# Kernel tuning notes

Measured on AMD Instinct MI355X. Metric: run time of the kernel, lower is better.

The kernel has to match this reference:

```python
import jax, jax.numpy as jnp
import numpy as np

B, S, W = 32, 256, 32
T = 16               # topics per doc, each spanning L = S//T sentences
VOCAB, E, H, D = 400001, 300, 128, 128


def _gru_scan(x, Wih, Whh, bih, bhh, reverse=False):
    """x: [B,S,E] -> (outputs [B,S,H], final hidden [B,H]). Torch GRU cell math."""
    h0 = jnp.zeros((x.shape[0], Whh.shape[1]), x.dtype)
    gi_all = jnp.einsum('bse,ge->bsg', x, Wih) + bih  # precompute input gates [B,S,3H]

    def step(h, gi):
        gh = h @ Whh.T + bhh
        ir, iz, inn = jnp.split(gi, 3, axis=-1)
        hr, hz, hn = jnp.split(gh, 3, axis=-1)
        r = jax.nn.sigmoid(ir + hr)
        z = jax.nn.sigmoid(iz + hz)
        n = jnp.tanh(inn + r * hn)
        h_new = (1.0 - z) * n + z * h
        return h_new, h_new

    hT, hs = jax.lax.scan(step, h0, jnp.swapaxes(gi_all, 0, 1), reverse=reverse)
    return jnp.swapaxes(hs, 0, 1), hT


def setup_inputs() -> dict:
    key = jax.random.key(0)
    ks = jax.random.split(key, 16)
    sc_i = 1.0 / np.sqrt(H)
    L = S // T
    starts = (jnp.arange(T, dtype=jnp.int32) * L + 1)          # 1-based inclusive
    ends = (jnp.arange(T, dtype=jnp.int32) + 1) * L
    tse = jnp.broadcast_to(jnp.stack([starts, ends], axis=-1)[None], (B, T, 2)).astype(jnp.int32)
    return {
        'word_ids': jax.random.randint(ks[0], (B, S, W), 0, VOCAB, dtype=jnp.int32),
        'topic_start_ends': tse,
        'embed_table': jax.random.normal(ks[1], (VOCAB, E), jnp.float32) * 0.6,
        'Wih_f': jax.random.normal(ks[2], (3 * H, E), jnp.float32) * sc_i,
        'Whh_f': jax.random.normal(ks[3], (3 * H, H), jnp.float32) * sc_i,
        'bih_f': jax.random.normal(ks[4], (3 * H,), jnp.float32) * sc_i,
        'bhh_f': jax.random.normal(ks[5], (3 * H,), jnp.float32) * sc_i,
        'Wih_b': jax.random.normal(ks[6], (3 * H, E), jnp.float32) * sc_i,
        'Whh_b': jax.random.normal(ks[7], (3 * H, H), jnp.float32) * sc_i,
        'bih_b': jax.random.normal(ks[8], (3 * H,), jnp.float32) * sc_i,
        'bhh_b': jax.random.normal(ks[9], (3 * H,), jnp.float32) * sc_i,
        'v_attention': jax.random.normal(ks[10], (4 * H, 1), jnp.float32),
        'W_attention': jax.random.normal(ks[11], (4 * H, 4 * H), jnp.float32) * (1.0 / np.sqrt(4 * H)),
        'W1': jax.random.normal(ks[12], (D, 4 * H), jnp.float32) * (1.0 / np.sqrt(4 * H)),
        'b1': jax.random.normal(ks[13], (D,), jnp.float32) * 0.01,
        'W2': jax.random.normal(ks[14], (1, D), jnp.float32) * (1.0 / np.sqrt(D)),
        'b2': jax.random.normal(ks[15], (1,), jnp.float32) * 0.01,
    }


def reference(word_ids, topic_start_ends, embed_table,
              Wih_f, Whh_f, bih_f, bhh_f, Wih_b, Whh_b, bih_b, bhh_b,
              v_attention, W_attention, W1, b1, W2, b2):
    b, s, _ = word_ids.shape
    h = Whh_f.shape[1]
    # --- sent_encoder: gather word embeddings, mean-pool per sentence ---
    sent_emb = jnp.mean(embed_table[word_ids], axis=2)          # [B,S,E]
    # --- doc_encoder: bi-GRU ---
    out_f, hT_f = _gru_scan(sent_emb, Wih_f, Whh_f, bih_f, bhh_f, reverse=False)
    out_b, hT_b = _gru_scan(sent_emb, Wih_b, Whh_b, bih_b, bhh_b, reverse=True)
    sent_rep = jnp.concatenate([out_f, out_b], axis=-1)         # [B,S,2H]
    # faithful to hidden.view(batch_size, 2H) on hidden of shape [2,B,H]
    doc_vec = jnp.stack([hT_f, hT_b], axis=0).reshape(b, 2 * h)
    doc_rep = jnp.broadcast_to(doc_vec[:, None, :], (b, s, 2 * h))
    # topic reps via segment difference of cumulative GRU states (pad trick)
    pad = jnp.pad(sent_rep, ((0, 0), (1, 1), (0, 0)))           # [B,S+2,2H]
    starts = topic_start_ends[:, :, 0]                          # [B,T], 1-based
    ends = topic_start_ends[:, :, 1]

    def gat(idx, lo, hi):
        return jnp.take_along_axis(pad[..., lo:hi], idx[:, :, None], axis=1)
    fwd_part = gat(ends, 0, h) - gat(starts - 1, 0, h)
    bwd_part = gat(starts, h, 2 * h) - gat(ends + 1, h, 2 * h)
    topic_mat = jnp.concatenate([fwd_part, bwd_part], axis=-1)  # [B,T,2H]
    # scatter topic vectors to sentences: topic id = #starts at or before sentence
    sidx = jnp.arange(s, dtype=starts.dtype)
    topic_id = jnp.sum(sidx[None, :, None] >= (starts - 1)[:, None, :], axis=-1) - 1  # [B,S]
    topic_rep = jnp.take_along_axis(topic_mat, topic_id[:, :, None], axis=1)          # [B,S,2H]
    # --- decoder ---
    cat_ds = jnp.concatenate([doc_rep, sent_rep], axis=-1)      # [B,S,4H]
    cat_ts = jnp.concatenate([topic_rep, sent_rep], axis=-1)
    doc_scores = jnp.tanh(cat_ds @ W_attention) @ v_attention   # [B,S,1]
    topic_scores = jnp.tanh(cat_ts @ W_attention) @ v_attention
    doc_w = jax.nn.softmax(doc_scores, axis=1)
    topic_w = jax.nn.softmax(topic_scores, axis=1)
    context = doc_w * doc_rep + topic_w * topic_rep             # [B,S,2H]
    inp = jnp.concatenate([sent_rep, context], axis=-1)         # [B,S,4H]
    hdd = jax.nn.relu(inp @ W1.T + b1)                          # dropout = identity (eval)
    logits = (hdd @ W2.T + b2).squeeze(-1)                      # [B,S]
    return logits
```

## Files before the change

### kernel.cpp

```cpp
#include <hip/hip_runtime.h>
#include <hip/hip_bf16.h>
#include <cstdint>

#define Bk 32
#define Sk 256
#define Wk 32
#define Tk 16
#define Ek 300
#define Hk 128
#define Dk 128
#define NROWS (Bk*Sk)
#define GI_N  (3*Hk*2)
#define KPAD  320

typedef __attribute__((ext_vector_type(8))) short short8v;
typedef __attribute__((ext_vector_type(4))) float f32x4;

__device__ __forceinline__ float fast_sigmoid(float x) {
    return 1.f / (1.f + __expf(-x));
}
__device__ __forceinline__ float fast_tanh(float x) {
    float ax = fabsf(x);
    float e = __expf(2.f * ax);
    float t = 1.f - 2.f / (1.f + e);
    return copysignf(t, x);
}
__device__ __forceinline__ void barrier_lgkm() {
    asm volatile("s_waitcnt lgkmcnt(0)" ::: "memory");
    __builtin_amdgcn_s_barrier();
}
__device__ __forceinline__ unsigned short f2bf(float f) {
    uint32_t u = __float_as_uint(f);
    uint32_t r = (u + 0x7FFFu + ((u >> 16) & 1u)) >> 16;
    return (unsigned short)r;
}
__device__ __forceinline__ float bf2f(unsigned short h) {
    return __uint_as_float(((uint32_t)h) << 16);
}

__global__ __launch_bounds__(256) void pack_kernel(
    const float* __restrict__ Wf, const float* __restrict__ Wb,
    const float* __restrict__ bf, const float* __restrict__ bb,
    const float* __restrict__ Watt, const float* __restrict__ W1,
    unsigned short* __restrict__ Bgt_hi, unsigned short* __restrict__ Bgt_lo,
    float* __restrict__ bias_gi, unsigned short* __restrict__ Wswt,
    unsigned short* __restrict__ W1H, unsigned short* __restrict__ W1L,
    unsigned short* __restrict__ WatTopH, unsigned short* __restrict__ WatTopL)
{
    int idx = blockIdx.x * 256 + threadIdx.x;
    if (idx < 768 * KPAD) {
        int n = idx / KPAD, k = idx % KPAD;
        float v = 0.f;
        if (k < 300) v = (n < 384) ? Wf[n * 300 + k] : Wb[(n - 384) * 300 + k];
        unsigned short h = f2bf(v);
        Bgt_hi[idx] = h;
        Bgt_lo[idx] = f2bf(v - bf2f(h));
    }
    if (idx < 768) bias_gi[idx] = (idx < 384) ? bf[idx] : bb[idx - 384];
    if (idx < 512 * 256) {
        int n = idx >> 8, k = idx & 255;
        Wswt[idx] = f2bf(Watt[(size_t)(256 + k) * 512 + n]);
        float v = Watt[(size_t)k * 512 + n];
        unsigned short h = f2bf(v);
        WatTopH[idx] = h;
        WatTopL[idx] = f2bf(v - bf2f(h));
    }
    if (idx < 128 * 512) {
        float v = W1[idx];
        unsigned short h = f2bf(v);
        W1H[idx] = h;
        W1L[idx] = f2bf(v - bf2f(h));
    }
}

__global__ __launch_bounds__(256) void embed_mean_kernel(
    const int* __restrict__ wids, const float* __restrict__ table,
    unsigned short* __restrict__ Ahi, unsigned short* __restrict__ Alo)
{
    int wv = (blockIdx.x << 2) + (threadIdx.x >> 6);
    int lane = threadIdx.x & 63;
    if (wv >= NROWS) return;
    const int* idp = wids + (size_t)wv * Wk;
    float4 a0 = {0,0,0,0}, a1 = {0,0,0,0};
    #pragma unroll 4
    for (int w = 0; w < Wk; ++w) {
        int id = idp[w];
        const float4* r4 = reinterpret_cast<const float4*>(table + (size_t)id * Ek);
        float4 v0 = r4[lane];
        a0.x += v0.x; a0.y += v0.y; a0.z += v0.z; a0.w += v0.w;
        if (lane < 11) {
            float4 v1 = r4[64 + lane];
            a1.x += v1.x; a1.y += v1.y; a1.z += v1.z; a1.w += v1.w;
        }
    }
    const float sc = 1.f / 32.f;
    unsigned short* hp = Ahi + (size_t)wv * KPAD;
    unsigned short* lp = Alo + (size_t)wv * KPAD;
    {
        float v[4] = {a0.x*sc, a0.y*sc, a0.z*sc, a0.w*sc};
        ushort4 h, l;
        h.x=f2bf(v[0]); h.y=f2bf(v[1]); h.z=f2bf(v[2]); h.w=f2bf(v[3]);
        l.x=f2bf(v[0]-bf2f(h.x)); l.y=f2bf(v[1]-bf2f(h.y));
        l.z=f2bf(v[2]-bf2f(h.z)); l.w=f2bf(v[3]-bf2f(h.w));
        *reinterpret_cast<ushort4*>(hp + lane*4) = h;
        *reinterpret_cast<ushort4*>(lp + lane*4) = l;
    }
    if (lane < 11) {
        float v[4] = {a1.x*sc, a1.y*sc, a1.z*sc, a1.w*sc};
        ushort4 h, l;
        h.x=f2bf(v[0]); h.y=f2bf(v[1]); h.z=f2bf(v[2]); h.w=f2bf(v[3]);
        l.x=f2bf(v[0]-bf2f(h.x)); l.y=f2bf(v[1]-bf2f(h.y));
        l.z=f2bf(v[2]-bf2f(h.z)); l.w=f2bf(v[3]-bf2f(h.w));
        *reinterpret_cast<ushort4*>(hp + 256 + lane*4) = h;
        *reinterpret_cast<ushort4*>(lp + 256 + lane*4) = l;
    } else if (lane < 16) {
        ushort4 z = {0,0,0,0};
        *reinterpret_cast<ushort4*>(hp + 256 + lane*4) = z;
        *reinterpret_cast<ushort4*>(lp + 256 + lane*4) = z;
    }
}

template<int PASSES, bool BIAS, bool RELU>
__global__ __launch_bounds__(256) void mfma_gemm_kernel(
    const unsigned short* __restrict__ Ahi, const unsigned short* __restrict__ Alo,
    const unsigned short* __restrict__ Bthi, const unsigned short* __restrict__ Btlo,
    const float* __restrict__ bias, float* __restrict__ C,
    int M, int N, int Kp)
{
    __shared__ unsigned short At_h[128][40];
    __shared__ unsigned short Bt_h[128][40];
    __shared__ unsigned short At_l[128][40];
    __shared__ unsigned short Bt_l[128][40];
    const int tid = threadIdx.x;
    const int m0 = blockIdx.x * 128, n0 = blockIdx.y * 128;
    const int lane = tid & 63;
    const int wave = tid >> 6;
    const int wr = (wave >> 1) * 64, wc = (wave & 1) * 64;
    const int l15 = lane & 15, l4 = lane >> 4;
    f32x4 acc[4][4] = {};

    const int srow = tid >> 1;
    const int scol = (tid & 1) * 16;

    for (int k0 = 0; k0 < Kp; k0 += 32) {
        {
            const unsigned short* ag = Ahi + (size_t)(m0 + srow) * Kp + k0 + scol;
            *reinterpret_cast<short8v*>(&At_h[srow][scol])     = *reinterpret_cast<const short8v*>(ag);
            *reinterpret_cast<short8v*>(&At_h[srow][scol + 8]) = *reinterpret_cast<const short8v*>(ag + 8);
            const unsigned short* bg = Bthi + (size_t)(n0 + srow) * Kp + k0 + scol;
            *reinterpret_cast<short8v*>(&Bt_h[srow][scol])     = *reinterpret_cast<const short8v*>(bg);
            *reinterpret_cast<short8v*>(&Bt_h[srow][scol + 8]) = *reinterpret_cast<const short8v*>(bg + 8);
            if (PASSES > 1) {
                const unsigned short* ag2 = Alo + (size_t)(m0 + srow) * Kp + k0 + scol;
                *reinterpret_cast<short8v*>(&At_l[srow][scol])     = *reinterpret_cast<const short8v*>(ag2);
                *reinterpret_cast<short8v*>(&At_l[srow][scol + 8]) = *reinterpret_cast<const short8v*>(ag2 + 8);
                const unsigned short* bg2 = Btlo + (size_t)(n0 + srow) * Kp + k0 + scol;
                *reinterpret_cast<short8v*>(&Bt_l[srow][scol])     = *reinterpret_cast<const short8v*>(bg2);
                *reinterpret_cast<short8v*>(&Bt_l[srow][scol + 8]) = *reinterpret_cast<const short8v*>(bg2 + 8);
            }
        }
        __syncthreads();
        short8v a_h[4], b_h[4], a_l[4], b_l[4];
        #pragma unroll
        for (int f = 0; f < 4; ++f) {
            a_h[f] = *reinterpret_cast<const short8v*>(&At_h[wr + f*16 + l15][l4*8]);
            b_h[f] = *reinterpret_cast<const short8v*>(&Bt_h[wc + f*16 + l15][l4*8]);
            if (PASSES > 1) {
                a_l[f] = *reinterpret_cast<const short8v*>(&At_l[wr + f*16 + l15][l4*8]);
                b_l[f] = *reinterpret_cast<const short8v*>(&Bt_l[wc + f*16 + l15][l4*8]);
            }
        }
        #pragma unroll
        for (int i = 0; i < 4; ++i) {
            #pragma unroll
            for (int j = 0; j < 4; ++j) {
                acc[i][j] = __builtin_amdgcn_mfma_f32_16x16x32_bf16(a_h[i], b_h[j], acc[i][j], 0, 0, 0);
                if (PASSES > 1) {
                    acc[i][j] = __builtin_amdgcn_mfma_f32_16x16x32_bf16(a_l[i], b_h[j], acc[i][j], 0, 0, 0);
                    acc[i][j] = __builtin_amdgcn_mfma_f32_16x16x32_bf16(a_h[i], b_l[j], acc[i][j], 0, 0, 0);
                }
            }
        }
        __syncthreads();
    }
    #pragma unroll
    for (int i = 0; i < 4; ++i) {
        #pragma unroll
        for (int j = 0; j < 4; ++j) {
            int col = n0 + wc + j * 16 + l15;
            float badd = BIAS ? bias[col] : 0.f;
            #pragma unroll
            for (int r = 0; r < 4; ++r) {
                int row = m0 + wr + i * 16 + l4 * 4 + r;
                float v = acc[i][j][r] + badd;
                if (RELU) v = fmaxf(v, 0.f);
                C[(size_t)row * N + col] = v;
            }
        }
    }
}

__global__ __launch_bounds__(256) void mfma_w1_logits_kernel(
    const unsigned short* __restrict__ Ahi, const unsigned short* __restrict__ Alo,
    const unsigned short* __restrict__ Bthi, const unsigned short* __restrict__ Btlo,
    const float* __restrict__ b1, const float* __restrict__ W2,
    const float* __restrict__ b2, float* __restrict__ out)
{
    __shared__ unsigned short At_h[128][40];
    __shared__ unsigned short Bt_h[128][40];
    __shared__ unsigned short At_l[128][40];
    __shared__ unsigned short Bt_l[128][40];
    __shared__ float lpart[128];
    const int Kp = 512;
    const int tid = threadIdx.x;
    const int m0 = blockIdx.x * 128;
    const int lane = tid & 63;
    const int wave = tid >> 6;
    const int wr = (wave >> 1) * 64, wc = (wave & 1) * 64;
    const int l15 = lane & 15, l4 = lane >> 4;
    f32x4 acc[4][4] = {};

    const int srow = tid >> 1;
    const int scol = (tid & 1) * 16;

    for (int k0 = 0; k0 < Kp; k0 += 32) {
        {
            const unsigned short* ag = Ahi + (size_t)(m0 + srow) * Kp + k0 + scol;
            *reinterpret_cast<short8v*>(&At_h[srow][scol])     = *reinterpret_cast<const short8v*>(ag);
            *reinterpret_cast<short8v*>(&At_h[srow][scol + 8]) = *reinterpret_cast<const short8v*>(ag + 8);
            const unsigned short* bg = Bthi + (size_t)srow * Kp + k0 + scol;
            *reinterpret_cast<short8v*>(&Bt_h[srow][scol])     = *reinterpret_cast<const short8v*>(bg);
            *reinterpret_cast<short8v*>(&Bt_h[srow][scol + 8]) = *reinterpret_cast<const short8v*>(bg + 8);
            const unsigned short* ag2 = Alo + (size_t)(m0 + srow) * Kp + k0 + scol;
            *reinterpret_cast<short8v*>(&At_l[srow][scol])     = *reinterpret_cast<const short8v*>(ag2);
            *reinterpret_cast<short8v*>(&At_l[srow][scol + 8]) = *reinterpret_cast<const short8v*>(ag2 + 8);
            const unsigned short* bg2 = Btlo + (size_t)srow * Kp + k0 + scol;
            *reinterpret_cast<short8v*>(&Bt_l[srow][scol])     = *reinterpret_cast<const short8v*>(bg2);
            *reinterpret_cast<short8v*>(&Bt_l[srow][scol + 8]) = *reinterpret_cast<const short8v*>(bg2 + 8);
        }
        __syncthreads();
        short8v a_h[4], b_h[4], a_l[4], b_l[4];
        #pragma unroll
        for (int f = 0; f < 4; ++f) {
            a_h[f] = *reinterpret_cast<const short8v*>(&At_h[wr + f*16 + l15][l4*8]);
            b_h[f] = *reinterpret_cast<const short8v*>(&Bt_h[wc + f*16 + l15][l4*8]);
            a_l[f] = *reinterpret_cast<const short8v*>(&At_l[wr + f*16 + l15][l4*8]);
            b_l[f] = *reinterpret_cast<const short8v*>(&Bt_l[wc + f*16 + l15][l4*8]);
        }
        #pragma unroll
        for (int i = 0; i < 4; ++i) {
            #pragma unroll
            for (int j = 0; j < 4; ++j) {
                acc[i][j] = __builtin_amdgcn_mfma_f32_16x16x32_bf16(a_h[i], b_h[j], acc[i][j], 0, 0, 0);
                acc[i][j] = __builtin_amdgcn_mfma_f32_16x16x32_bf16(a_l[i], b_h[j], acc[i][j], 0, 0, 0);
                acc[i][j] = __builtin_amdgcn_mfma_f32_16x16x32_bf16(a_h[i], b_l[j], acc[i][j], 0, 0, 0);
            }
        }
        __syncthreads();
    }
    float b1v[4], w2v[4];
    #pragma unroll
    for (int j = 0; j < 4; ++j) {
        int col = wc + j * 16 + l15;
        b1v[j] = b1[col];
        w2v[j] = W2[col];
    }
    float lsum[4][4];
    #pragma unroll
    for (int i = 0; i < 4; ++i) {
        #pragma unroll
        for (int r = 0; r < 4; ++r) {
            float s = 0.f;
            #pragma unroll
            for (int j = 0; j < 4; ++j) {
                float v = fmaxf(acc[i][j][r] + b1v[j], 0.f);
                s = fmaf(v, w2v[j], s);
            }
            s += __shfl_xor(s, 1); s += __shfl_xor(s, 2);
            s += __shfl_xor(s, 4); s += __shfl_xor(s, 8);
            lsum[i][r] = s;
        }
    }
    if (wc == 0 && l15 == 0) {
        #pragma unroll
        for (int i = 0; i < 4; ++i)
            #pragma unroll
            for (int r = 0; r < 4; ++r)
                lpart[wr + i * 16 + l4 * 4 + r] = lsum[i][r];
    }
    __syncthreads();
    if (wc == 64 && l15 == 0) {
        float bb2 = b2[0];
        #pragma unroll
        for (int i = 0; i < 4; ++i)
            #pragma unroll
            for (int r = 0; r < 4; ++r) {
                int rl = wr + i * 16 + l4 * 4 + r;
                out[m0 + rl] = lpart[rl] + lsum[i][r] + bb2;
            }
    }
}

__global__ __launch_bounds__(256) void mfma_swscore_kernel(
    const unsigned short* __restrict__ Ahi, const unsigned short* __restrict__ Bthi,
    const float* __restrict__ dptp, const float* __restrict__ vatt,
    const int* __restrict__ tidmap,
    float* __restrict__ dscp, float* __restrict__ tscp)
{
    __shared__ unsigned short At_h[128][40];
    __shared__ unsigned short Bt_h[128][40];
    const int tid = threadIdx.x;
    const int m0 = blockIdx.x * 128, n0 = blockIdx.y * 128;
    const int Kp = 256;
    const int lane = tid & 63;
    const int wave = tid >> 6;
    const int wr = (wave >> 1) * 64, wc = (wave & 1) * 64;
    const int l15 = lane & 15, l4 = lane >> 4;
    f32x4 acc[4][4] = {};

    const int srow = tid >> 1;
    const int scol = (tid & 1) * 16;

    for (int k0 = 0; k0 < Kp; k0 += 32) {
        {
            const unsigned short* ag = Ahi + (size_t)(m0 + srow) * Kp + k0 + scol;
            *reinterpret_cast<short8v*>(&At_h[srow][scol])     = *reinterpret_cast<const short8v*>(ag);
            *reinterpret_cast<short8v*>(&At_h[srow][scol + 8]) = *reinterpret_cast<const short8v*>(ag + 8);
            const unsigned short* bg = Bthi + (size_t)(n0 + srow) * Kp + k0 + scol;
            *reinterpret_cast<short8v*>(&Bt_h[srow][scol])     = *reinterpret_cast<const short8v*>(bg);
            *reinterpret_cast<short8v*>(&Bt_h[srow][scol + 8]) = *reinterpret_cast<const short8v*>(bg + 8);
        }
        __syncthreads();
        short8v a_h[4], b_h[4];
        #pragma unroll
        for (int f = 0; f < 4; ++f) {
            a_h[f] = *reinterpret_cast<const short8v*>(&At_h[wr + f*16 + l15][l4*8]);
            b_h[f] = *reinterpret_cast<const short8v*>(&Bt_h[wc + f*16 + l15][l4*8]);
        }
        #pragma unroll
        for (int i = 0; i < 4; ++i)
            #pragma unroll
            for (int j = 0; j < 4; ++j)
                acc[i][j] = __builtin_amdgcn_mfma_f32_16x16x32_bf16(a_h[i], b_h[j], acc[i][j], 0, 0, 0);
        __syncthreads();
    }
    const int bb = m0 >> 8;
    const float* dpr = dptp + (size_t)bb * 512;
    float vv[4], dpv[4];
    #pragma unroll
    for (int j = 0; j < 4; ++j) {
        int col = n0 + wc + j * 16 + l15;
        vv[j] = vatt[col];
        dpv[j] = dpr[col];
    }
    const int slot = blockIdx.y * 2 + (wc >> 6);
    #pragma unroll
    for (int i = 0; i < 4; ++i) {
        #pragma unroll
        for (int r = 0; r < 4; ++r) {
            int row = m0 + wr + i * 16 + l4 * 4 + r;
            int ti = tidmap[row];
            const float* tpr = dptp + (size_t)(32 + bb * 16 + ti) * 512;
            float sd = 0.f, st = 0.f;
            #pragma unroll
            for (int j = 0; j < 4; ++j) {
                int col = n0 + wc + j * 16 + l15;
                float c = acc[i][j][r];
                sd += fast_tanh(c + dpv[j]) * vv[j];
                st += fast_tanh(c + tpr[col]) * vv[j];
            }
            sd += __shfl_xor(sd, 1); sd += __shfl_xor(sd, 2);
            sd += __shfl_xor(sd, 4); sd += __shfl_xor(sd, 8);
            st += __shfl_xor(st, 1); st += __shfl_xor(st, 2);
            st += __shfl_xor(st, 4); st += __shfl_xor(st, 8);
            if (l15 == 0) {
                dscp[(size_t)row * 8 + slot] = sd;
                tscp[(size_t)row * 8 + slot] = st;
            }
        }
    }
}

__global__ __launch_bounds__(512, 1) void gru_scan_kernel(
    const float* __restrict__ gi,
    const float* __restrict__ Whh_f, const float* __restrict__ Whh_b,
    const float* __restrict__ bhh_f, const float* __restrict__ bhh_b,
    float* __restrict__ sent_rep, unsigned short* __restrict__ srh,
    float* __restrict__ hT)
{
    const int blk = blockIdx.x;
    const int dir = blk >> 5;
    const int b   = blk & 31;
    const int t = threadIdx.x;
    const int lane = t & 63;
    const int w_id = t >> 6;
    const int q = lane >> 4;
    const int m = lane & 15;
    const int j = w_id * 16 + m;
    const float* Whh = dir ? Whh_b : Whh_f;
    const float* bhh = dir ? bhh_b : bhh_f;
    __shared__ float hbufA[144];
    __shared__ float hbufB[144];

    const float* wr0 = Whh + (size_t)j * 128 + 32 * q;
    const float* wr1 = wr0 + 128 * 128;
    const float* wr2 = wr0 + 256 * 128;
    float4 wA0 = *reinterpret_cast<const float4*>(wr0 +  0);
    float4 wA1 = *reinterpret_cast<const float4*>(wr0 +  4);
    float4 wA2 = *reinterpret_cast<const float4*>(wr0 +  8);
    float4 wA3 = *reinterpret_cast<const float4*>(wr0 + 12);
    float4 wA4 = *reinterpret_cast<const float4*>(wr0 + 16);
    float4 wA5 = *reinterpret_cast<const float4*>(wr0 + 20);
    float4 wA6 = *reinterpret_cast<const float4*>(wr0 + 24);
    float4 wA7 = *reinterpret_cast<const float4*>(wr0 + 28);
    float4 wB0 = *reinterpret_cast<const float4*>(wr1 +  0);
    float4 wB1 = *reinterpret_cast<const float4*>(wr1 +  4);
    float4 wB2 = *reinterpret_cast<const float4*>(wr1 +  8);
    float4 wB3 = *reinterpret_cast<const float4*>(wr1 + 12);
    float4 wB4 = *reinterpret_cast<const float4*>(wr1 + 16);
    float4 wB5 = *reinterpret_cast<const float4*>(wr1 + 20);
    float4 wB6 = *reinterpret_cast<const float4*>(wr1 + 24);
    float4 wB7 = *reinterpret_cast<const float4*>(wr1 + 28);
    float4 wC0 = *reinterpret_cast<const float4*>(wr2 +  0);
    float4 wC1 = *reinterpret_cast<const float4*>(wr2 +  4);
    float4 wC2 = *reinterpret_cast<const float4*>(wr2 +  8);
    float4 wC3 = *reinterpret_cast<const float4*>(wr2 + 12);
    float4 wC4 = *reinterpret_cast<const float4*>(wr2 + 16);
    float4 wC5 = *reinterpret_cast<const float4*>(wr2 + 20);
    float4 wC6 = *reinterpret_cast<const float4*>(wr2 + 24);
    float4 wC7 = *reinterpret_cast<const float4*>(wr2 + 28);
    const float br = bhh[j];
    const float bz = bhh[128 + j];
    const float bn = bhh[256 + j];

    if (t < 144) { hbufA[t] = 0.f; hbufB[t] = 0.f; }

    const int ji = 36 * (j >> 5) + (j & 31);
    const float* gbase = gi + (size_t)(b * Sk) * GI_N + dir * 384 + j;
    float hold = 0.f;
    float ar = 0.f, az = 0.f, an_ = 0.f;
    float brr = 0.f, bzz = 0.f, bnn = 0.f;
    {
        const long s0 = dir ? (Sk - 1) : 0;
        const long s1 = dir ? (Sk - 2) : 1;
        const float* g0 = gbase + s0 * GI_N;
        ar = g0[0]; az = g0[128]; an_ = g0[256];
        const float* g1 = gbase + s1 * GI_N;
        brr = g1[0]; bzz = g1[128]; bnn = g1[256];
    }
    __syncthreads();

    #define STEP(RD, WR, SEXPR, GR, GZ, GN, SAVE) { \
        const int s = (SEXPR); \
        const float4* hseg = reinterpret_cast<const float4*>(RD) + 9 * q; \
        float pA = 0.f, pB = 0.f, pC = 0.f; \
        { float4 h4; \
          h4 = hseg[0]; \
          pA=fmaf(wA0.x,h4.x,pA); pA=fmaf(wA0.y,h4.y,pA); pA=fmaf(wA0.z,h4.z,pA); pA=fmaf(wA0.w,h4.w,pA); \
          pB=fmaf(wB0.x,h4.x,pB); pB=fmaf(wB0.y,h4.y,pB); pB=fmaf(wB0.z,h4.z,pB); pB=fmaf(wB0.w,h4.w,pB); \
          pC=fmaf(wC0.x,h4.x,pC); pC=fmaf(wC0.y,h4.y,pC); pC=fmaf(wC0.z,h4.z,pC); pC=fmaf(wC0.w,h4.w,pC); \
          h4 = hseg[1]; \
          pA=fmaf(wA1.x,h4.x,pA); pA=fmaf(wA1.y,h4.y,pA); pA=fmaf(wA1.z,h4.z,pA); pA=fmaf(wA1.w,h4.w,pA); \
          pB=fmaf(wB1.x,h4.x,pB); pB=fmaf(wB1.y,h4.y,pB); pB=fmaf(wB1.z,h4.z,pB); pB=fmaf(wB1.w,h4.w,pB); \
          pC=fmaf(wC1.x,h4.x,pC); pC=fmaf(wC1.y,h4.y,pC); pC=fmaf(wC1.z,h4.z,pC); pC=fmaf(wC1.w,h4.w,pC); \
          h4 = hseg[2]; \
          pA=fmaf(wA2.x,h4.x,pA); pA=fmaf(wA2.y,h4.y,pA); pA=fmaf(wA2.z,h4.z,pA); pA=fmaf(wA2.w,h4.w,pA); \
          pB=fmaf(wB2.x,h4.x,pB); pB=fmaf(wB2.y,h4.y,pB); pB=fmaf(wB2.z,h4.z,pB); pB=fmaf(wB2.w,h4.w,pB); \
          pC=fmaf(wC2.x,h4.x,pC); pC=fmaf(wC2.y,h4.y,pC); pC=fmaf(wC2.z,h4.z,pC); pC=fmaf(wC2.w,h4.w,pC); \
          h4 = hseg[3]; \
          pA=fmaf(wA3.x,h4.x,pA); pA=fmaf(wA3.y,h4.y,pA); pA=fmaf(wA3.z,h4.z,pA); pA=fmaf(wA3.w,h4.w,pA); \
          pB=fmaf(wB3.x,h4.x,pB); pB=fmaf(wB3.y,h4.y,pB); pB=fmaf(wB3.z,h4.z,pB); pB=fmaf(wB3.w,h4.w,pB); \
          pC=fmaf(wC3.x,h4.x,pC); pC=fmaf(wC3.y,h4.y,pC); pC=fmaf(wC3.z,h4.z,pC); pC=fmaf(wC3.w,h4.w,pC); \
          h4 = hseg[4]; \
          pA=fmaf(wA4.x,h4.x,pA); pA=fmaf(wA4.y,h4.y,pA); pA=fmaf(wA4.z,h4.z,pA); pA=fmaf(wA4.w,h4.w,pA); \
          pB=fmaf(wB4.x,h4.x,pB); pB=fmaf(wB4.y,h4.y,pB); pB=fmaf(wB4.z,h4.z,pB); pB=fmaf(wB4.w,h4.w,pB); \
          pC=fmaf(wC4.x,h4.x,pC); pC=fmaf(wC4.y,h4.y,pC); pC=fmaf(wC4.z,h4.z,pC); pC=fmaf(wC4.w,h4.w,pC); \
          h4 = hseg[5]; \
          pA=fmaf(wA5.x,h4.x,pA); pA=fmaf(wA5.y,h4.y,pA); pA=fmaf(wA5.z,h4.z,pA); pA=fmaf(wA5.w,h4.w,pA); \
          pB=fmaf(wB5.x,h4.x,pB); pB=fmaf(wB5.y,h4.y,pB); pB=fmaf(wB5.z,h4.z,pB); pB=fmaf(wB5.w,h4.w,pB); \
          pC=fmaf(wC5.x,h4.x,pC); pC=fmaf(wC5.y,h4.y,pC); pC=fmaf(wC5.z,h4.z,pC); pC=fmaf(wC5.w,h4.w,pC); \
          h4 = hseg[6]; \
          pA=fmaf(wA6.x,h4.x,pA); pA=fmaf(wA6.y,h4.y,pA); pA=fmaf(wA6.z,h4.z,pA); pA=fmaf(wA6.w,h4.w,pA); \
          pB=fmaf(wB6.x,h4.x,pB); pB=fmaf(wB6.y,h4.y,pB); pB=fmaf(wB6.z,h4.z,pB); pB=fmaf(wB6.w,h4.w,pB); \
          pC=fmaf(wC6.x,h4.x,pC); pC=fmaf(wC6.y,h4.y,pC); pC=fmaf(wC6.z,h4.z,pC); pC=fmaf(wC6.w,h4.w,pC); \
          h4 = hseg[7]; \
          pA=fmaf(wA7.x,h4.x,pA); pA=fmaf(wA7.y,h4.y,pA); pA=fmaf(wA7.z,h4.z,pA); pA=fmaf(wA7.w,h4.w,pA); \
          pB=fmaf(wB7.x,h4.x,pB); pB=fmaf(wB7.y,h4.y,pB); pB=fmaf(wB7.z,h4.z,pB); pB=fmaf(wB7.w,h4.w,pB); \
          pC=fmaf(wC7.x,h4.x,pC); pC=fmaf(wC7.y,h4.y,pC); pC=fmaf(wC7.z,h4.z,pC); pC=fmaf(wC7.w,h4.w,pC); } \
        pA += __shfl_xor(pA, 16); pA += __shfl_xor(pA, 32); \
        pB += __shfl_xor(pB, 16); pB += __shfl_xor(pB, 32); \
        pC += __shfl_xor(pC, 16); pC += __shfl_xor(pC, 32); \
        if (q == 0) { \
            float r = fast_sigmoid(GR + pA + br); \
            float z = fast_sigmoid(GZ + pB + bz); \
            float n = fast_tanh(GN + r * (pC + bn)); \
            hold = (1.f - z) * n + z * hold; \
            (WR)[ji] = hold; \
            SAVE = hold; \
            const long sn = dir ? (long)s - 2 : (long)s + 2; \
            const float* gp = gbase + sn * GI_N; \
            GR = gp[0]; GZ = gp[128]; GN = gp[256]; \
        } \
        barrier_lgkm(); \
    }

    for (int step = 0; step < Sk; step += 4) {
        float h0 = 0.f, h1 = 0.f, h2 = 0.f, h3 = 0.f;
        STEP(hbufA, hbufB, dir ? (Sk - 1 - step) : step,       ar, az, an_, h0);
        STEP(hbufB, hbufA, dir ? (Sk - 2 - step) : (step + 1), brr, bzz, bnn, h1);
        STEP(hbufA, hbufB, dir ? (Sk - 3 - step) : (step + 2), ar, az, an_, h2);
        STEP(hbufB, hbufA, dir ? (Sk - 4 - step) : (step + 3), brr, bzz, bnn, h3);
        if (q == 0) {
            const size_t base = (size_t)(b * Sk) * 256 + dir * 128 + j;
            const int sA = dir ? (Sk - 1 - step) : step;
            const int d1 = dir ? -1 : 1;
            sent_rep[base + (size_t)(sA)          * 256] = h0;
            sent_rep[base + (size_t)(sA + d1)     * 256] = h1;
            sent_rep[base + (size_t)(sA + 2 * d1) * 256] = h2;
            sent_rep[base + (size_t)(sA + 3 * d1) * 256] = h3;
            srh[base + (size_t)(sA)          * 256] = f2bf(h0);
            srh[base + (size_t)(sA + d1)     * 256] = f2bf(h1);
            srh[base + (size_t)(sA + 2 * d1) * 256] = f2bf(h2);
            srh[base + (size_t)(sA + 3 * d1) * 256] = f2bf(h3);
        }
    }
    #undef STEP

    if (q == 0) hT[dir * 4096 + b * 128 + j] = hold;
}

__device__ __forceinline__ float4 sr_load_guard(const float* sr, int b, int sidx, int j4) {
    if (sidx < 0 || sidx >= Sk) { float4 z = {0,0,0,0}; return z; }
    return reinterpret_cast<const float4*>(sr)[(size_t)(b * Sk + sidx) * 64 + j4];
}
__global__ __launch_bounds__(64) void prep_kernel(
    const int* __restrict__ tse, const float* __restrict__ sent_rep,
    const float* __restrict__ hT, float* __restrict__ dvtm,
    unsigned short* __restrict__ dvtmH, unsigned short* __restrict__ dvtmL,
    int* __restrict__ tidmap)
{
    const int b = blockIdx.x;
    const int t = blockIdx.y;
    const int j4 = threadIdx.x;
    float4 v;
    int row;
    if (t == 16) {
        int dir = b >> 4;
        int bb = 2 * (b & 15) + (j4 >> 5);
        int jj4 = j4 & 31;
        v = reinterpret_cast<const float4*>(hT)[dir * 1024 + bb * 32 + jj4];
        row = b;
        for (int ss = j4; ss < 256; ss += 64) {
            int ti = 0;
            #pragma unroll
            for (int tt = 1; tt < 16; ++tt) ti += (ss >= tse[b * 32 + tt * 2] - 1) ? 1 : 0;
            tidmap[b * 256 + ss] = ti;
        }
    } else {
        int st = tse[b * 32 + t * 2];
        int en = tse[b * 32 + t * 2 + 1];
        float4 va, vb;
        if (j4 < 32) {
            va = sr_load_guard(sent_rep, b, en - 1, j4);
            vb = sr_load_guard(sent_rep, b, st - 2, j4);
        } else {
            va = sr_load_guard(sent_rep, b, st - 1, j4);
            vb = sr_load_guard(sent_rep, b, en, j4);
        }
        v.x = va.x - vb.x; v.y = va.y - vb.y; v.z = va.z - vb.z; v.w = va.w - vb.w;
        row = 32 + b * 16 + t;
    }
    reinterpret_cast<float4*>(dvtm)[row * 64 + j4] = v;
    ushort4 h, l;
    h.x = f2bf(v.x); h.y = f2bf(v.y); h.z = f2bf(v.z); h.w = f2bf(v.w);
    l.x = f2bf(v.x - bf2f(h.x)); l.y = f2bf(v.y - bf2f(h.y));
    l.z = f2bf(v.z - bf2f(h.z)); l.w = f2bf(v.w - bf2f(h.w));
    *reinterpret_cast<ushort4*>(dvtmH + (size_t)row * 256 + j4 * 4) = h;
    *reinterpret_cast<ushort4*>(dvtmL + (size_t)row * 256 + j4 * 4) = l;
}

__global__ __launch_bounds__(256) void softmax_kernel(
    const float* __restrict__ dscp, const float* __restrict__ tscp,
    float* __restrict__ dsc, float* __restrict__ tsc)
{
    const int b = blockIdx.x, sidx = threadIdx.x;
    const int lane = sidx & 63, wid = sidx >> 6;
    __shared__ float rd[4], rt[4];
    const float4* dp8 = reinterpret_cast<const float4*>(dscp + (size_t)(b * Sk + sidx) * 8);
    const float4* tp8 = reinterpret_cast<const float4*>(tscp + (size_t)(b * Sk + sidx) * 8);
    float4 d0 = dp8[0], d1 = dp8[1], t0 = tp8[0], t1 = tp8[1];
    float d = ((d0.x + d0.y) + (d0.z + d0.w)) + ((d1.x + d1.y) + (d1.z + d1.w));
    float t = ((t0.x + t0.y) + (t0.z + t0.w)) + ((t1.x + t1.y) + (t1.z + t1.w));
    float md = d, mt = t;
    #pragma unroll
    for (int off = 32; off; off >>= 1) {
        md = fmaxf(md, __shfl_xor(md, off));
        mt = fmaxf(mt, __shfl_xor(mt, off));
    }
    if (lane == 0) { rd[wid] = md; rt[wid] = mt; }
    __syncthreads();
    md = fmaxf(fmaxf(rd[0], rd[1]), fmaxf(rd[2], rd[3]));
    mt = fmaxf(fmaxf(rt[0], rt[1]), fmaxf(rt[2], rt[3]));
    float ed = __expf(d - md), et = __expf(t - mt);
    float sd = ed, stt = et;
    #pragma unroll
    for (int off = 32; off; off >>= 1) {
        sd += __shfl_xor(sd, off);
        stt += __shfl_xor(stt, off);
    }
    __syncthreads();
    if (lane == 0) { rd[wid] = sd; rt[wid] = stt; }
    __syncthreads();
    sd = rd[0] + rd[1] + rd[2] + rd[3];
    stt = rt[0] + rt[1] + rt[2] + rt[3];
    dsc[b * Sk + sidx] = ed / sd;
    tsc[b * Sk + sidx] = et / stt;
}

__global__ __launch_bounds__(128) void build_inp_kernel(
    const float* __restrict__ sent_rep, const float* __restrict__ dvtm,
    const float* __restrict__ dw, const float* __restrict__ tw,
    const int* __restrict__ tidmap,
    unsigned short* __restrict__ inpH, unsigned short* __restrict__ inpL)
{
    int row = blockIdx.x;
    int b = row >> 8;
    int f4c = threadIdx.x;
    float4 v;
    if (f4c < 64) {
        v = reinterpret_cast<const float4*>(sent_rep)[(size_t)row * 64 + f4c];
    } else {
        int ti = tidmap[row];
        float dwv = dw[row], twv = tw[row];
        int j4 = f4c - 64;
        float4 dv = reinterpret_cast<const float4*>(dvtm)[b * 64 + j4];
        float4 tm = reinterpret_cast<const float4*>(dvtm)[(32 + b * 16 + ti) * 64 + j4];
        v.x = dwv * dv.x + twv * tm.x;
        v.y = dwv * dv.y + twv * tm.y;
        v.z = dwv * dv.z + twv * tm.z;
        v.w = dwv * dv.w + twv * tm.w;
    }
    ushort4 h, l;
    h.x = f2bf(v.x); h.y = f2bf(v.y); h.z = f2bf(v.z); h.w = f2bf(v.w);
    l.x = f2bf(v.x - bf2f(h.x)); l.y = f2bf(v.y - bf2f(h.y));
    l.z = f2bf(v.z - bf2f(h.z)); l.w = f2bf(v.w - bf2f(h.w));
    *reinterpret_cast<ushort4*>(inpH + (size_t)row * 512 + f4c * 4) = h;
    *reinterpret_cast<ushort4*>(inpL + (size_t)row * 512 + f4c * 4) = l;
}

extern "C" void kernel_launch(void* const* d_in, const int* in_sizes, int n_in,
                              void* d_out, int out_size, void* d_ws, size_t ws_size,
                              hipStream_t stream)
{
    const int*   wids  = (const int*)d_in[0];
    const int*   tse   = (const int*)d_in[1];
    const float* table = (const float*)d_in[2];
    const float* Wihf  = (const float*)d_in[3];
    const float* Whhf  = (const float*)d_in[4];
    const float* bihf  = (const float*)d_in[5];
    const float* bhhf  = (const float*)d_in[6];
    const float* Wihb  = (const float*)d_in[7];
    const float* Whhb  = (const float*)d_in[8];
    const float* bihb  = (const float*)d_in[9];
    const float* bhhb  = (const float*)d_in[10];
    const float* vatt  = (const float*)d_in[11];
    const float* Watt  = (const float*)d_in[12];
    const float* W1    = (const float*)d_in[13];
    const float* b1    = (const float*)d_in[14];
    const float* W2    = (const float*)d_in[15];
    const float* b2    = (const float*)d_in[16];
    float* ws = (float*)d_ws;
    float* out = (float*)d_out;

    unsigned short* Ahi   = (unsigned short*)(ws + 0);
    unsigned short* Alo   = (unsigned short*)(ws + 1310720);
    float* gi             = ws + 2621440;
    float* sent_rep       = ws + 8912896;
    unsigned short* SRhi  = (unsigned short*)(ws + 11010048);
    float* hT             = ws + 12058624;
    float* dvtm           = ws + 12066816;
    float* dptp           = ws + 12206080;
    float* dsc            = ws + 12533760;
    float* tsc            = ws + 12541952;
    unsigned short* BgtH  = (unsigned short*)(ws + 12550144);
    unsigned short* BgtL  = (unsigned short*)(ws + 12673024);
    float* bias_gi        = ws + 12795904;
    unsigned short* Wswt  = (unsigned short*)(ws + 12796672);
    unsigned short* W1H   = (unsigned short*)(ws + 12862208);
    unsigned short* W1L   = (unsigned short*)(ws + 12894976);
    float* dscp           = ws + 12927744;
    float* tscp           = ws + 12993280;
    int*   tidmap         = (int*)(ws + 13058816);
    unsigned short* dvtmH = (unsigned short*)(ws + 13067008);
    unsigned short* dvtmL = (unsigned short*)(ws + 13148928);
    unsigned short* WatTH = (unsigned short*)(ws + 13230848);
    unsigned short* WatTL = (unsigned short*)(ws + 13296384);
    unsigned short* inpH  = (unsigned short*)(ws + 0);
    unsigned short* inpL  = (unsigned short*)(ws + 2097152);

    if (ws_size < (size_t)13361920 * sizeof(float)) return;

    pack_kernel<<<960, 256, 0, stream>>>(Wihf, Wihb, bihf, bihb, Watt, W1,
                                         BgtH, BgtL, bias_gi, Wswt, W1H, W1L,
                                         WatTH, WatTL);
    embed_mean_kernel<<<2048, 256, 0, stream>>>(wids, table, Ahi, Alo);
    mfma_gemm_kernel<3, true, false><<<dim3(64, 6), 256, 0, stream>>>(
        Ahi, Alo, BgtH, BgtL, bias_gi, gi, NROWS, 768, KPAD);
    gru_scan_kernel<<<64, 512, 0, stream>>>(gi, Whhf, Whhb, bhhf, bhhb,
                                            sent_rep, SRhi, hT);
    prep_kernel<<<dim3(32, 17), 64, 0, stream>>>(tse, sent_rep, hT, dvtm,
                                                 dvtmH, dvtmL, tidmap);
    mfma_gemm_kernel<3, false, false><<<dim3(5, 4), 256, 0, stream>>>(
        dvtmH, dvtmL, WatTH, WatTL, nullptr, dptp, 640, 512, 256);
    mfma_swscore_kernel<<<dim3(64, 4), 256, 0, stream>>>(
        SRhi, Wswt, dptp, vatt, tidmap, dscp, tscp);
    softmax_kernel<<<32, 256, 0, stream>>>(dscp, tscp, dsc, tsc);
    build_inp_kernel<<<NROWS, 128, 0, stream>>>(sent_rep, dvtm, dsc, tsc, tidmap, inpH, inpL);
    mfma_w1_logits_kernel<<<dim3(64, 1), 256, 0, stream>>>(
        inpH, inpL, W1H, W1L, b1, W2, b2, out);
}
```

Baseline: 332.6 us.

## Batch GRU recurrence across 16 sequences per block using split-bf16 MFMA

The GRU scan kernel is rewritten so that each of four blocks handles one direction and 16 batch rows. The per-step h·Whh^T product runs on MFMA bf16 instructions, with hi/lo splitting of both h and Whh to keep near-fp32 accuracy. The previous scalar FMA kernel used 64 blocks, one per (direction, batch) pair. The change cuts redundant weight work per step but leaves only four blocks active for the serial 256-step chain, so each step now carries MFMA latency, LDS round trips and strided global gi loads.

```diff
diff --git a/kernel.cpp b/kernel.cpp
--- a/kernel.cpp
+++ b/kernel.cpp
@@ -40,12 +40,14 @@
 
 __global__ __launch_bounds__(256) void pack_kernel(
     const float* __restrict__ Wf, const float* __restrict__ Wb,
+    const float* __restrict__ Whh_f, const float* __restrict__ Whh_b,
     const float* __restrict__ bf, const float* __restrict__ bb,
     const float* __restrict__ Watt, const float* __restrict__ W1,
     unsigned short* __restrict__ Bgt_hi, unsigned short* __restrict__ Bgt_lo,
     float* __restrict__ bias_gi, unsigned short* __restrict__ Wswt,
     unsigned short* __restrict__ W1H, unsigned short* __restrict__ W1L,
-    unsigned short* __restrict__ WatTopH, unsigned short* __restrict__ WatTopL)
+    unsigned short* __restrict__ WatTopH, unsigned short* __restrict__ WatTopL,
+    unsigned short* __restrict__ WhhH, unsigned short* __restrict__ WhhL)
 {
     int idx = blockIdx.x * 256 + threadIdx.x;
     if (idx < 768 * KPAD) {
@@ -70,6 +72,15 @@
         unsigned short h = f2bf(v);
         W1H[idx] = h;
         W1L[idx] = f2bf(v - bf2f(h));
+    }
+    if (idx < 2 * 384 * 128) {
+        int dd = idx / 49152;
+        int rest = idx - dd * 49152;
+        const float* W = dd ? Whh_b : Whh_f;
+        float v = W[rest];
+        unsigned short h = f2bf(v);
+        WhhH[idx] = h;
+        WhhL[idx] = f2bf(v - bf2f(h));
     }
 }
 
@@ -381,152 +392,109 @@
     }
 }
 
-__global__ __launch_bounds__(512, 1) void gru_scan_kernel(
+__global__ __launch_bounds__(512, 1) void gru_scan_mfma_kernel(
     const float* __restrict__ gi,
-    const float* __restrict__ Whh_f, const float* __restrict__ Whh_b,
+    const unsigned short* __restrict__ WhhH, const unsigned short* __restrict__ WhhL,
     const float* __restrict__ bhh_f, const float* __restrict__ bhh_b,
     float* __restrict__ sent_rep, unsigned short* __restrict__ srh,
     float* __restrict__ hT)
 {
-    const int blk = blockIdx.x;
-    const int dir = blk >> 5;
-    const int b   = blk & 31;
+    const int dir  = blockIdx.x >> 1;
+    const int half = blockIdx.x & 1;
     const int t = threadIdx.x;
     const int lane = t & 63;
-    const int w_id = t >> 6;
-    const int q = lane >> 4;
-    const int m = lane & 15;
-    const int j = w_id * 16 + m;
-    const float* Whh = dir ? Whh_b : Whh_f;
+    const int w = t >> 6;
+    const int l15 = lane & 15, l4 = lane >> 4;
+    const int j = w * 16 + l15;
     const float* bhh = dir ? bhh_b : bhh_f;
-    __shared__ float hbufA[144];
-    __shared__ float hbufB[144];
-
-    const float* wr0 = Whh + (size_t)j * 128 + 32 * q;
-    const float* wr1 = wr0 + 128 * 128;
-    const float* wr2 = wr0 + 256 * 128;
-    float4 wA0 = *reinterpret_cast<const float4*>(wr0 +  0);
-    float4 wA1 = *reinterpret_cast<const float4*>(wr0 +  4);
-    float4 wA2 = *reinterpret_cast<const float4*>(wr0 +  8);
-    float4 wA3 = *reinterpret_cast<const float4*>(wr0 + 12);
-    float4 wA4 = *reinterpret_cast<const float4*>(wr0 + 16);
-    float4 wA5 = *reinterpret_cast<const float4*>(wr0 + 20);
-    float4 wA6 = *reinterpret_cast<const float4*>(wr0 + 24);
-    float4 wA7 = *reinterpret_cast<const float4*>(wr0 + 28);
-    float4 wB0 = *reinterpret_cast<const float4*>(wr1 +  0);
-    float4 wB1 = *reinterpret_cast<const float4*>(wr1 +  4);
-    float4 wB2 = *reinterpret_cast<const float4*>(wr1 +  8);
-    float4 wB3 = *reinterpret_cast<const float4*>(wr1 + 12);
-    float4 wB4 = *reinterpret_cast<const float4*>(wr1 + 16);
-    float4 wB5 = *reinterpret_cast<const float4*>(wr1 + 20);
-    float4 wB6 = *reinterpret_cast<const float4*>(wr1 + 24);
-    float4 wB7 = *reinterpret_cast<const float4*>(wr1 + 28);
-    float4 wC0 = *reinterpret_cast<const float4*>(wr2 +  0);
-    float4 wC1 = *reinterpret_cast<const float4*>(wr2 +  4);
-    float4 wC2 = *reinterpret_cast<const float4*>(wr2 +  8);
-    float4 wC3 = *reinterpret_cast<const float4*>(wr2 + 12);
-    float4 wC4 = *reinterpret_cast<const float4*>(wr2 + 16);
-    float4 wC5 = *reinterpret_cast<const float4*>(wr2 + 20);
-    float4 wC6 = *reinterpret_cast<const float4*>(wr2 + 24);
-    float4 wC7 = *reinterpret_cast<const float4*>(wr2 + 28);
-    const float br = bhh[j];
-    const float bz = bhh[128 + j];
-    const float bn = bhh[256 + j];
-
-    if (t < 144) { hbufA[t] = 0.f; hbufB[t] = 0.f; }
-
-    const int ji = 36 * (j >> 5) + (j & 31);
-    const float* gbase = gi + (size_t)(b * Sk) * GI_N + dir * 384 + j;
-    float hold = 0.f;
-    float ar = 0.f, az = 0.f, an_ = 0.f;
-    float brr = 0.f, bzz = 0.f, bnn = 0.f;
+    __shared__ unsigned short hls[2][2][16][152];
+
+    const unsigned short* WH = WhhH + (size_t)dir * 49152;
+    const unsigned short* WL = WhhL + (size_t)dir * 49152;
+    short8v bh0[4], bh1[4], bh2[4], bl0[4], bl1[4], bl2[4];
+    #pragma unroll
+    for (int kt = 0; kt < 4; ++kt) {
+        const size_t ko = (size_t)kt * 32 + l4 * 8;
+        bh0[kt] = *reinterpret_cast<const short8v*>(WH + (size_t)(0 * 128 + j) * 128 + ko);
+        bh1[kt] = *reinterpret_cast<const short8v*>(WH + (size_t)(1 * 128 + j) * 128 + ko);
+        bh2[kt] = *reinterpret_cast<const short8v*>(WH + (size_t)(2 * 128 + j) * 128 + ko);
+        bl0[kt] = *reinterpret_cast<const short8v*>(WL + (size_t)(0 * 128 + j) * 128 + ko);
+        bl1[kt] = *reinterpret_cast<const short8v*>(WL + (size_t)(1 * 128 + j) * 128 + ko);
+        bl2[kt] = *reinterpret_cast<const short8v*>(WL + (size_t)(2 * 128 + j) * 128 + ko);
+    }
+    const float b_r = bhh[j], b_z = bhh[128 + j], b_n = bhh[256 + j];
+
+    for (int i = t; i < 2 * 2 * 16 * 152; i += 512) ((unsigned short*)hls)[i] = 0;
+
+    float giA[12], giB[12];
     {
-        const long s0 = dir ? (Sk - 1) : 0;
-        const long s1 = dir ? (Sk - 2) : 1;
-        const float* g0 = gbase + s0 * GI_N;
-        ar = g0[0]; az = g0[128]; an_ = g0[256];
-        const float* g1 = gbase + s1 * GI_N;
-        brr = g1[0]; bzz = g1[128]; bnn = g1[256];
-    }
+        const int s0 = dir ? (Sk - 1) : 0;
+        const int s1 = dir ? (Sk - 2) : 1;
+        #pragma unroll
+        for (int r = 0; r < 4; ++r) {
+            const int b = half * 16 + l4 * 4 + r;
+            const float* g0 = gi + ((size_t)b * Sk + s0) * GI_N + dir * 384 + j;
+            giA[3*r+0] = g0[0]; giA[3*r+1] = g0[128]; giA[3*r+2] = g0[256];
+            const float* g1 = gi + ((size_t)b * Sk + s1) * GI_N + dir * 384 + j;
+            giB[3*r+0] = g1[0]; giB[3*r+1] = g1[128]; giB[3*r+2] = g1[256];
+        }
+    }
+    float hprev[4] = {0.f, 0.f, 0.f, 0.f};
     __syncthreads();
 
-    #define STEP(RD, WR, SEXPR, GR, GZ, GN, SAVE) { \
+    int cur = 0;
+    #define SSTEP(GIBUF, SEXPR) { \
         const int s = (SEXPR); \
-        const float4* hseg = reinterpret_cast<const float4*>(RD) + 9 * q; \
-        float pA = 0.f, pB = 0.f, pC = 0.f; \
-        { float4 h4; \
-          h4 = hseg[0]; \
-          pA=fmaf(wA0.x,h4.x,pA); pA=fmaf(wA0.y,h4.y,pA); pA=fmaf(wA0.z,h4.z,pA); pA=fmaf(wA0.w,h4.w,pA); \
-          pB=fmaf(wB0.x,h4.x,pB); pB=fmaf(wB0.y,h4.y,pB); pB=fmaf(wB0.z,h4.z,pB); pB=fmaf(wB0.w,h4.w,pB); \
-          pC=fmaf(wC0.x,h4.x,pC); pC=fmaf(wC0.y,h4.y,pC); pC=fmaf(wC0.z,h4.z,pC); pC=fmaf(wC0.w,h4.w,pC); \
-          h4 = hseg[1]; \
-          pA=fmaf(wA1.x,h4.x,pA); pA=fmaf(wA1.y,h4.y,pA); pA=fmaf(wA1.z,h4.z,pA); pA=fmaf(wA1.w,h4.w,pA); \
-          pB=fmaf(wB1.x,h4.x,pB); pB=fmaf(wB1.y,h4.y,pB); pB=fmaf(wB1.z,h4.z,pB); pB=fmaf(wB1.w,h4.w,pB); \
-          pC=fmaf(wC1.x,h4.x,pC); pC=fmaf(wC1.y,h4.y,pC); pC=fmaf(wC1.z,h4.z,pC); pC=fmaf(wC1.w,h4.w,pC); \
-          h4 = hseg[2]; \
-          pA=fmaf(wA2.x,h4.x,pA); pA=fmaf(wA2.y,h4.y,pA); pA=fmaf(wA2.z,h4.z,pA); pA=fmaf(wA2.w,h4.w,pA); \
-          pB=fmaf(wB2.x,h4.x,pB); pB=fmaf(wB2.y,h4.y,pB); pB=fmaf(wB2.z,h4.z,pB); pB=fmaf(wB2.w,h4.w,pB); \
-          pC=fmaf(wC2.x,h4.x,pC); pC=fmaf(wC2.y,h4.y,pC); pC=fmaf(wC2.z,h4.z,pC); pC=fmaf(wC2.w,h4.w,pC); \
-          h4 = hseg[3]; \
-          pA=fmaf(wA3.x,h4.x,pA); pA=fmaf(wA3.y,h4.y,pA); pA=fmaf(wA3.z,h4.z,pA); pA=fmaf(wA3.w,h4.w,pA); \
-          pB=fmaf(wB3.x,h4.x,pB); pB=fmaf(wB3.y,h4.y,pB); pB=fmaf(wB3.z,h4.z,pB); pB=fmaf(wB3.w,h4.w,pB); \
-          pC=fmaf(wC3.x,h4.x,pC); pC=fmaf(wC3.y,h4.y,pC); pC=fmaf(wC3.z,h4.z,pC); pC=fmaf(wC3.w,h4.w,pC); \
-          h4 = hseg[4]; \
-          pA=fmaf(wA4.x,h4.x,pA); pA=fmaf(wA4.y,h4.y,pA); pA=fmaf(wA4.z,h4.z,pA); pA=fmaf(wA4.w,h4.w,pA); \
-          pB=fmaf(wB4.x,h4.x,pB); pB=fmaf(wB4.y,h4.y,pB); pB=fmaf(wB4.z,h4.z,pB); pB=fmaf(wB4.w,h4.w,pB); \
-          pC=fmaf(wC4.x,h4.x,pC); pC=fmaf(wC4.y,h4.y,pC); pC=fmaf(wC4.z,h4.z,pC); pC=fmaf(wC4.w,h4.w,pC); \
-          h4 = hseg[5]; \
-          pA=fmaf(wA5.x,h4.x,pA); pA=fmaf(wA5.y,h4.y,pA); pA=fmaf(wA5.z,h4.z,pA); pA=fmaf(wA5.w,h4.w,pA); \
-          pB=fmaf(wB5.x,h4.x,pB); pB=fmaf(wB5.y,h4.y,pB); pB=fmaf(wB5.z,h4.z,pB); pB=fmaf(wB5.w,h4.w,pB); \
-          pC=fmaf(wC5.x,h4.x,pC); pC=fmaf(wC5.y,h4.y,pC); pC=fmaf(wC5.z,h4.z,pC); pC=fmaf(wC5.w,h4.w,pC); \
-          h4 = hseg[6]; \
-          pA=fmaf(wA6.x,h4.x,pA); pA=fmaf(wA6.y,h4.y,pA); pA=fmaf(wA6.z,h4.z,pA); pA=fmaf(wA6.w,h4.w,pA); \
-          pB=fmaf(wB6.x,h4.x,pB); pB=fmaf(wB6.y,h4.y,pB); pB=fmaf(wB6.z,h4.z,pB); pB=fmaf(wB6.w,h4.w,pB); \
-          pC=fmaf(wC6.x,h4.x,pC); pC=fmaf(wC6.y,h4.y,pC); pC=fmaf(wC6.z,h4.z,pC); pC=fmaf(wC6.w,h4.w,pC); \
-          h4 = hseg[7]; \
-          pA=fmaf(wA7.x,h4.x,pA); pA=fmaf(wA7.y,h4.y,pA); pA=fmaf(wA7.z,h4.z,pA); pA=fmaf(wA7.w,h4.w,pA); \
-          pB=fmaf(wB7.x,h4.x,pB); pB=fmaf(wB7.y,h4.y,pB); pB=fmaf(wB7.z,h4.z,pB); pB=fmaf(wB7.w,h4.w,pB); \
-          pC=fmaf(wC7.x,h4.x,pC); pC=fmaf(wC7.y,h4.y,pC); pC=fmaf(wC7.z,h4.z,pC); pC=fmaf(wC7.w,h4.w,pC); } \
-        pA += __shfl_xor(pA, 16); pA += __shfl_xor(pA, 32); \
-        pB += __shfl_xor(pB, 16); pB += __shfl_xor(pB, 32); \
-        pC += __shfl_xor(pC, 16); pC += __shfl_xor(pC, 32); \
-        if (q == 0) { \
-            float r = fast_sigmoid(GR + pA + br); \
-            float z = fast_sigmoid(GZ + pB + bz); \
-            float n = fast_tanh(GN + r * (pC + bn)); \
-            hold = (1.f - z) * n + z * hold; \
-            (WR)[ji] = hold; \
-            SAVE = hold; \
+        short8v ah[4], al[4]; \
+        _Pragma("unroll") \
+        for (int kt = 0; kt < 4; ++kt) { \
+            ah[kt] = *reinterpret_cast<const short8v*>(&hls[cur][0][l15][kt*32 + l4*8]); \
+            al[kt] = *reinterpret_cast<const short8v*>(&hls[cur][1][l15][kt*32 + l4*8]); \
+        } \
+        f32x4 accR = {}, accZ = {}, accN = {}; \
+        _Pragma("unroll") \
+        for (int kt = 0; kt < 4; ++kt) { \
+            accR = __builtin_amdgcn_mfma_f32_16x16x32_bf16(ah[kt], bh0[kt], accR, 0, 0, 0); \
+            accR = __builtin_amdgcn_mfma_f32_16x16x32_bf16(al[kt], bh0[kt], accR, 0, 0, 0); \
+            accR = __builtin_amdgcn_mfma_f32_16x16x32_bf16(ah[kt], bl0[kt], accR, 0, 0, 0); \
+            accZ = __builtin_amdgcn_mfma_f32_16x16x32_bf16(ah[kt], bh1[kt], accZ, 0, 0, 0); \
+            accZ = __builtin_amdgcn_mfma_f32_16x16x32_bf16(al[kt], bh1[kt], accZ, 0, 0, 0); \
+            accZ = __builtin_amdgcn_mfma_f32_16x16x32_bf16(ah[kt], bl1[kt], accZ, 0, 0, 0); \
+            accN = __builtin_amdgcn_mfma_f32_16x16x32_bf16(ah[kt], bh2[kt], accN, 0, 0, 0); \
+            accN = __builtin_amdgcn_mfma_f32_16x16x32_bf16(al[kt], bh2[kt], accN, 0, 0, 0); \
+            accN = __builtin_amdgcn_mfma_f32_16x16x32_bf16(ah[kt], bl2[kt], accN, 0, 0, 0); \
+        } \
+        const int nxt = cur ^ 1; \
+        _Pragma("unroll") \
+        for (int r = 0; r < 4; ++r) { \
+            float rr = fast_sigmoid(GIBUF[3*r+0] + accR[r] + b_r); \
+            float zz = fast_sigmoid(GIBUF[3*r+1] + accZ[r] + b_z); \
+            float nn = fast_tanh(GIBUF[3*r+2] + rr * (accN[r] + b_n)); \
+            float hnew = (1.f - zz) * nn + zz * hprev[r]; \
+            hprev[r] = hnew; \
+            const size_t orow = ((size_t)(half*16 + l4*4 + r) * Sk + s); \
+            sent_rep[orow * 256 + dir * 128 + j] = hnew; \
+            srh[orow * 256 + dir * 128 + j] = f2bf(hnew); \
+            unsigned short hh = f2bf(hnew); \
+            hls[nxt][0][l4*4 + r][j] = hh; \
+            hls[nxt][1][l4*4 + r][j] = f2bf(hnew - bf2f(hh)); \
             const long sn = dir ? (long)s - 2 : (long)s + 2; \
-            const float* gp = gbase + sn * GI_N; \
-            GR = gp[0]; GZ = gp[128]; GN = gp[256]; \
+            const float* gp = gi + ((long)(half*16 + l4*4 + r) * Sk + sn) * GI_N + dir * 384 + j; \
+            GIBUF[3*r+0] = gp[0]; GIBUF[3*r+1] = gp[128]; GIBUF[3*r+2] = gp[256]; \
         } \
         barrier_lgkm(); \
-    }
-
-    for (int step = 0; step < Sk; step += 4) {
-        float h0 = 0.f, h1 = 0.f, h2 = 0.f, h3 = 0.f;
-        STEP(hbufA, hbufB, dir ? (Sk - 1 - step) : step,       ar, az, an_, h0);
-        STEP(hbufB, hbufA, dir ? (Sk - 2 - step) : (step + 1), brr, bzz, bnn, h1);
-        STEP(hbufA, hbufB, dir ? (Sk - 3 - step) : (step + 2), ar, az, an_, h2);
-        STEP(hbufB, hbufA, dir ? (Sk - 4 - step) : (step + 3), brr, bzz, bnn, h3);
-        if (q == 0) {
-            const size_t base = (size_t)(b * Sk) * 256 + dir * 128 + j;
-            const int sA = dir ? (Sk - 1 - step) : step;
-            const int d1 = dir ? -1 : 1;
-            sent_rep[base + (size_t)(sA)          * 256] = h0;
-            sent_rep[base + (size_t)(sA + d1)     * 256] = h1;
-            sent_rep[base + (size_t)(sA + 2 * d1) * 256] = h2;
-            sent_rep[base + (size_t)(sA + 3 * d1) * 256] = h3;
-            srh[base + (size_t)(sA)          * 256] = f2bf(h0);
-            srh[base + (size_t)(sA + d1)     * 256] = f2bf(h1);
-            srh[base + (size_t)(sA + 2 * d1) * 256] = f2bf(h2);
-            srh[base + (size_t)(sA + 3 * d1) * 256] = f2bf(h3);
-        }
-    }
-    #undef STEP
-
-    if (q == 0) hT[dir * 4096 + b * 128 + j] = hold;
+        cur ^= 1; \
+    }
+
+    for (int step = 0; step < Sk; step += 2) {
+        SSTEP(giA, dir ? (Sk - 1 - step) : step);
+        SSTEP(giB, dir ? (Sk - 2 - step) : (step + 1));
+    }
+    #undef SSTEP
+
+    #pragma unroll
+    for (int r = 0; r < 4; ++r)
+        hT[dir * 4096 + (half * 16 + l4 * 4 + r) * 128 + j] = hprev[r];
 }
 
 __device__ __forceinline__ float4 sr_load_guard(const float* sr, int b, int sidx, int j4) {
@@ -695,19 +663,21 @@
     unsigned short* dvtmL = (unsigned short*)(ws + 13148928);
     unsigned short* WatTH = (unsigned short*)(ws + 13230848);
     unsigned short* WatTL = (unsigned short*)(ws + 13296384);
+    unsigned short* WhhHp = (unsigned short*)(ws + 13361920);
+    unsigned short* WhhLp = (unsigned short*)(ws + 13411072);
     unsigned short* inpH  = (unsigned short*)(ws + 0);
     unsigned short* inpL  = (unsigned short*)(ws + 2097152);
 
-    if (ws_size < (size_t)13361920 * sizeof(float)) return;
-
-    pack_kernel<<<960, 256, 0, stream>>>(Wihf, Wihb, bihf, bihb, Watt, W1,
-                                         BgtH, BgtL, bias_gi, Wswt, W1H, W1L,
-                                         WatTH, WatTL);
+    if (ws_size < (size_t)13460224 * sizeof(float)) return;
+
+    pack_kernel<<<960, 256, 0, stream>>>(Wihf, Wihb, Whhf, Whhb, bihf, bihb,
+                                         Watt, W1, BgtH, BgtL, bias_gi, Wswt,
+                                         W1H, W1L, WatTH, WatTL, WhhHp, WhhLp);
     embed_mean_kernel<<<2048, 256, 0, stream>>>(wids, table, Ahi, Alo);
     mfma_gemm_kernel<3, true, false><<<dim3(64, 6), 256, 0, stream>>>(
         Ahi, Alo, BgtH, BgtL, bias_gi, gi, NROWS, 768, KPAD);
-    gru_scan_kernel<<<64, 512, 0, stream>>>(gi, Whhf, Whhb, bhhf, bhhb,
-                                            sent_rep, SRhi, hT);
+    gru_scan_mfma_kernel<<<4, 512, 0, stream>>>(gi, WhhHp, WhhLp, bhhf, bhhb,
+                                                sent_rep, SRhi, hT);
     prep_kernel<<<dim3(32, 17), 64, 0, stream>>>(tse, sent_rep, hT, dvtm,
                                                  dvtmH, dvtmL, tidmap);
     mfma_gemm_kernel<3, false, false><<<dim3(5, 4), 256, 0, stream>>>(
```

New measurement: 563.6 us. +69.5%, slower.
